# Kernel optimization log

Hardware: AMD Instinct MI355X
Metric: run time of the kernel (lower is better)

Reference implementation:

```python
import jax, jax.numpy as jnp
import numpy as np


def setup_inputs() -> dict:
    key = jax.random.key(0)
    k1, k2, k3 = jax.random.split(key, 3)
    B, C, N, G, D = 64, 4, 1024, 32, 3
    patches = jax.random.normal(k1, (B, C, N, G, D), dtype=jnp.float32)
    centers = jax.random.normal(k2, (B, C, N, D), dtype=jnp.float32)
    # crops_centers_idx: uniform multinomial over n_patches, one per flat batch elem
    center_idx = jax.random.randint(k3, (B * C,), 0, N)
    # crop_length ~ randint(0.25*N, 0.75*N); fixed to midpoint 512 for static shapes
    return {"patches": patches, "centers": centers, "center_idx": center_idx, "K": 512}


def reference(patches, centers, center_idx, K):
    B, C, N, G, D = patches.shape
    BF = B * C
    # flatten (b, c) -> bf, matching PatchedCloud.flatten()
    p = patches.reshape(BF, N, G, D)
    c = centers.reshape(BF, N, D)
    # gather the sampled crop center per flat batch element: [BF, D]
    q = c[jnp.arange(BF), center_idx]
    # knn_points: squared L2 distances from query to all centers, K smallest (sorted)
    d2 = jnp.sum((q[:, None, :] - c) ** 2, axis=-1)  # [BF, N]
    _, idx = jax.lax.top_k(-d2, K)                   # [BF, K], ascending distance
    b = jnp.arange(BF)[:, None]
    cropped_patches = p[b, idx]   # [BF, K, G, D]
    cropped_centers = c[b, idx]   # [BF, K, D]
    return (cropped_patches.reshape(B, C, K, G, D),
            cropped_centers.reshape(B, C, K, D))
```

## Files before the change

kernel.cpp:

```cpp
#include <hip/hip_runtime.h>
#include <hip/hip_bf16.h>

#define BFN   256
#define NPTS  1024
#define KSEL  512
#define GD    96
#define ROW4  24

typedef unsigned long long u64;

__global__ __launch_bounds__(1024)
void sel_kernel(const float* __restrict__ centers,
                const int*   __restrict__ center_idx,
                int* __restrict__ rank_ws,
                float* __restrict__ out_centers)
{
    __shared__ u64 lds[NPTS];
    const int bf = blockIdx.x;
    const int t  = threadIdx.x;

    rank_ws[bf * NPTS + t] = -1;

    const float* cbase = centers + (size_t)bf * NPTS * 3;
    const int qi = center_idx[bf];
    const float q0 = cbase[qi * 3 + 0], q1 = cbase[qi * 3 + 1], q2 = cbase[qi * 3 + 2];
    const float c0 = cbase[t * 3 + 0],  c1 = cbase[t * 3 + 1],  c2 = cbase[t * 3 + 2];

    const double e0 = (double)q0 - (double)c0;
    const double e1 = (double)q1 - (double)c1;
    const double e2 = (double)q2 - (double)c2;
    const double d2 = e0 * e0 + e1 * e1 + e2 * e2;

    u64 key = (((u64)__double_as_longlong(d2)) & ~0x3FFull) | (u64)t;

    for (int size = 2; size <= NPTS; size <<= 1) {
        const bool dir = (t & size) != 0;
        for (int stride = size >> 1; stride > 0; stride >>= 1) {
            u64 other;
            if (stride >= 64) {
                __syncthreads();
                lds[t] = key;
                __syncthreads();
                other = lds[t ^ stride];
            } else {
                other = __shfl_xor(key, stride, 64);
            }
            const bool upper    = (t & stride) != 0;
            const bool keep_min = (upper == dir);
            const bool mine_lt  = key < other;
            key = (keep_min == mine_lt) ? key : other;
        }
    }
    __syncthreads();

    if (t < KSEL) {
        const int idx = (int)(key & 0x3FFull);
        rank_ws[bf * NPTS + idx] = t;
        const float* cs = cbase + (size_t)idx * 3;
        float* oc = out_centers + ((size_t)bf * KSEL + t) * 3;
        oc[0] = cs[0]; oc[1] = cs[1]; oc[2] = cs[2];
    }
}

__global__ __launch_bounds__(256)
void gather_kernel(const float4* __restrict__ patches4,
                   const int*    __restrict__ rank_ws,
                   float4*       __restrict__ out_p4)
{
    __shared__ int rank_s[256];
    const int b     = blockIdx.x;
    const int bf    = b >> 2;
    const int chunk = b & 3;
    const int t     = threadIdx.x;

    rank_s[t] = rank_ws[bf * NPTS + chunk * 256 + t];
    __syncthreads();

    const float4* src = patches4 + ((size_t)bf * NPTS + (size_t)chunk * 256) * ROW4;
    float4*       dst = out_p4   + (size_t)bf * KSEL * ROW4;

    #pragma unroll
    for (int it = 0; it < 24; ++it) {
        const int flat = it * 256 + t;
        const float4 v = src[flat];
        const int row  = flat / 24;
        const int lane = flat - row * 24;
        const int r    = rank_s[row];
        if (r >= 0) dst[(size_t)r * ROW4 + lane] = v;
    }
}

extern "C" void kernel_launch(void* const* d_in, const int* in_sizes, int n_in,
                              void* d_out, int out_size, void* d_ws, size_t ws_size,
                              hipStream_t stream)
{
    const float* patches    = (const float*)d_in[0];
    const float* centers    = (const float*)d_in[1];
    const int*   center_idx = (const int*)d_in[2];

    float* out_patches = (float*)d_out;
    float* out_centers = (float*)d_out + (size_t)BFN * KSEL * GD;
    int*   rank_ws     = (int*)d_ws;

    sel_kernel<<<BFN, 1024, 0, stream>>>(centers, center_idx, rank_ws, out_centers);
    gather_kernel<<<BFN * 4, 256, 0, stream>>>((const float4*)patches, rank_ws,
                                               (float4*)out_patches);
}
```

Measured before the change: 170.4 us.

## Fuse kNN selection and patch gather into one kernel with LDS rank map

Merges the sorting/selection kernel and the patch gather kernel into a single 1024-thread block per batch element. The rank map is kept in shared memory, so the global workspace round trip and the second launch go away. The cost is that the gather now runs in only 256 blocks, and it cannot overlap with sorting from other blocks the way the separate launch could. Each block still loads all 1024 patch rows and discards the unselected half.

```diff
diff --git a/kernel.cpp b/kernel.cpp
--- a/kernel.cpp
+++ b/kernel.cpp
@@ -10,16 +10,19 @@
 typedef unsigned long long u64;
 
 __global__ __launch_bounds__(1024)
-void sel_kernel(const float* __restrict__ centers,
-                const int*   __restrict__ center_idx,
-                int* __restrict__ rank_ws,
-                float* __restrict__ out_centers)
+void crop_fused_kernel(const float*  __restrict__ centers,
+                       const float4* __restrict__ patches4,
+                       const int*    __restrict__ center_idx,
+                       float4* __restrict__ out_p4,
+                       float*  __restrict__ out_c)
 {
-    __shared__ u64 lds[NPTS];
+    __shared__ u64 keys[NPTS];
+    __shared__ int rank_s[NPTS];
+
     const int bf = blockIdx.x;
     const int t  = threadIdx.x;
 
-    rank_ws[bf * NPTS + t] = -1;
+    rank_s[t] = -1;
 
     const float* cbase = centers + (size_t)bf * NPTS * 3;
     const int qi = center_idx[bf];
@@ -39,9 +42,9 @@
             u64 other;
             if (stride >= 64) {
                 __syncthreads();
-                lds[t] = key;
+                keys[t] = key;
                 __syncthreads();
-                other = lds[t ^ stride];
+                other = keys[t ^ stride];
             } else {
                 other = __shfl_xor(key, stride, 64);
             }
@@ -55,33 +58,19 @@
 
     if (t < KSEL) {
         const int idx = (int)(key & 0x3FFull);
-        rank_ws[bf * NPTS + idx] = t;
+        rank_s[idx] = t;
         const float* cs = cbase + (size_t)idx * 3;
-        float* oc = out_centers + ((size_t)bf * KSEL + t) * 3;
+        float* oc = out_c + ((size_t)bf * KSEL + t) * 3;
         oc[0] = cs[0]; oc[1] = cs[1]; oc[2] = cs[2];
     }
-}
-
-__global__ __launch_bounds__(256)
-void gather_kernel(const float4* __restrict__ patches4,
-                   const int*    __restrict__ rank_ws,
-                   float4*       __restrict__ out_p4)
-{
-    __shared__ int rank_s[256];
-    const int b     = blockIdx.x;
-    const int bf    = b >> 2;
-    const int chunk = b & 3;
-    const int t     = threadIdx.x;
-
-    rank_s[t] = rank_ws[bf * NPTS + chunk * 256 + t];
     __syncthreads();
 
-    const float4* src = patches4 + ((size_t)bf * NPTS + (size_t)chunk * 256) * ROW4;
+    const float4* src = patches4 + (size_t)bf * NPTS * ROW4;
     float4*       dst = out_p4   + (size_t)bf * KSEL * ROW4;
 
     #pragma unroll
     for (int it = 0; it < 24; ++it) {
-        const int flat = it * 256 + t;
+        const int flat = it * 1024 + t;
         const float4 v = src[flat];
         const int row  = flat / 24;
         const int lane = flat - row * 24;
@@ -100,9 +89,8 @@
 
     float* out_patches = (float*)d_out;
     float* out_centers = (float*)d_out + (size_t)BFN * KSEL * GD;
-    int*   rank_ws     = (int*)d_ws;
 
-    sel_kernel<<<BFN, 1024, 0, stream>>>(centers, center_idx, rank_ws, out_centers);
-    gather_kernel<<<BFN * 4, 256, 0, stream>>>((const float4*)patches, rank_ws,
-                                               (float4*)out_patches);
+    crop_fused_kernel<<<BFN, 1024, 0, stream>>>(centers, (const float4*)patches,
+                                                center_idx, (float4*)out_patches,
+                                                out_centers);
 }
```

Measured after the change: 170.6 us. No clear change (+0.1%).
